# Kernel optimization log

Hardware: AMD Instinct MI355X
Metric: run time of the kernel (lower is better)

The kernel has to match this reference:

```python
import jax, jax.numpy as jnp
import numpy as np

B, F, V, D = 16384, 16, 100000, 16  # batch, n_fields, vocab, embed_dim; dims = F*D = 256
EPS = 1e-5


def _bn(x, g, b):
    # torch.nn.BatchNorm1d in training mode: biased batch variance
    m = x.mean(0)
    v = x.var(0)
    return g * (x - m) * jax.lax.rsqrt(v + EPS) + b


def setup_inputs() -> dict:
    ks = iter(jax.random.split(jax.random.key(0), 40))

    def rn(shape, s=0.05):
        return jax.random.normal(next(ks), shape, jnp.float32) * s

    return {
        "feat_ids": jax.random.randint(next(ks), (B, F), 0, V, jnp.int32),
        "domain_ids": jax.random.randint(next(ks), (B,), 0, 3, jnp.int32),
        "emb": rn((F, V, D), 0.1),
        "hW0": rn((256, 128)), "hb0": jnp.zeros(128), "hg0": jnp.ones(128), "hbe0": jnp.zeros(128),
        "hW1": rn((128, 64)), "hb1": jnp.zeros(64), "hg1": jnp.ones(64), "hbe1": jnp.zeros(64),
        "hW2": rn((64, 1024)), "hb2": jnp.zeros(1024), "hg2": jnp.ones(1024), "hbe2": jnp.zeros(1024),
        "cw": rn((3, 256)), "cb": jnp.zeros((3, 256)),
        "mW0": rn((256, 512)), "mb0": jnp.zeros(512), "mg0": jnp.ones(512), "mbe0": jnp.zeros(512),
        "mW1": rn((512, 256)), "mb1": jnp.zeros(256), "mg1": jnp.ones(256), "mbe1": jnp.zeros(256),
        "u0": rn((256, 32)), "u1": rn((32, 32)), "v0": rn((32, 32)), "v1": rn((32, 256)),
        "ab0": jnp.zeros(32), "ab1": jnp.zeros(256),
        "gamma1": jnp.ones(256), "bias1": jnp.zeros(256),
        "lw": rn((512,)), "lb": jnp.zeros(1),
    }


def _forward(feat_ids, emb, hW0, hb0, hg0, hbe0, hW1, hb1, hg1, hbe1,
             hW2, hb2, hg2, hbe2, cw, cb, mW0, mb0, mg0, mbe0,
             mW1, mb1, mg1, mbe1, u0, u1, v0, v1, ab0, ab1,
             gamma1, bias1, lw, lb):
    b, f = feat_ids.shape
    # EmbeddingLayer(squeeze_dim=True): per-field lookup then concat -> [B, F*D]
    e = emb[jnp.arange(f)[None, :], feat_ids].reshape(b, -1)
    h = e
    for W, bb, g, be in ((hW0, hb0, hg0, hbe0), (hW1, hb1, hg1, hbe1), (hW2, hb2, hg2, hbe2)):
        h = jax.nn.relu(_bn(h @ W + bb, g, be))
    k = u1.shape[0]
    H = h.reshape(b, k, k)  # [B, k, k]
    # CrossNetwork: x_{l+1} = x0 * (x_l . w_l) + b_l + x_l
    x = e
    for i in range(cw.shape[0]):
        x = e * (x @ cw[i])[:, None] + cb[i] + x
    cn_out = x  # [B, 256]
    m = e
    for W, bb, g, be in ((mW0, mb0, mg0, mbe0), (mW1, mb1, mg1, mbe1)):
        m = jax.nn.relu(_bn(m @ W + bb, g, be))
    # hyper low-rank adapter: einsum('mi,bij,jn->bmn') applied lazily so the
    # [B,256,32] per-sample weight is never materialized (associativity)
    t = jax.nn.sigmoid(jnp.einsum('bi,bij->bj', m @ u0, H) @ v0 + ab0)   # [B, 32]
    t = jnp.einsum('bi,bij->bj', t @ u1, H) @ v1 + ab1                    # [B, 256]
    mu = t.mean(0)
    var = t.var(0, ddof=1)  # torch.var default is unbiased
    m = gamma1 * (t - mu) / jnp.sqrt(var + EPS) + bias1 + m  # norm + residual
    y = jnp.concatenate([cn_out, m], axis=1) @ lw + lb[0]     # LR head
    # Every domain branch computes identical values (shared weights, full-batch
    # input, dropout p=0), so the torch.where domain-select is the identity.
    return jax.nn.sigmoid(y)  # [B]


def reference(feat_ids, domain_ids, emb, hW0, hb0, hg0, hbe0, hW1, hb1, hg1, hbe1,
              hW2, hb2, hg2, hbe2, cw, cb, mW0, mb0, mg0, mbe0,
              mW1, mb1, mg1, mbe1, u0, u1, v0, v1, ab0, ab1,
              gamma1, bias1, lw, lb):
    return _forward(feat_ids, emb, hW0, hb0, hg0, hbe0, hW1, hb1, hg1, hbe1,
                    hW2, hb2, hg2, hbe2, cw, cb, mW0, mb0, mg0, mbe0,
                    mW1, mb1, mg1, mbe1, u0, u1, v0, v1, ab0, ab1,
                    gamma1, bias1, lw, lb)
```

## Files before the change

### kernel.cpp

```cpp
#include <hip/hip_runtime.h>

typedef unsigned short u16;
typedef __attribute__((ext_vector_type(8))) short bf16x8;
typedef __attribute__((ext_vector_type(4))) float f32x4;
#define BATCH 16384

__device__ __forceinline__ float b2f(u16 u){ unsigned int i=((unsigned int)u)<<16; float f; __builtin_memcpy(&f,&i,4); return f; }
__device__ __forceinline__ u16 f2b(float f){ unsigned int x; __builtin_memcpy(&x,&f,4); unsigned int r=(x + 0x7fffu + ((x>>16)&1u))>>16; return (u16)r; }

__global__ __launch_bounds__(256) void zero_kernel(float* __restrict__ p, int n){
  int i = blockIdx.x*256 + threadIdx.x;
  if (i < n) p[i] = 0.f;
}

__global__ __launch_bounds__(256) void transpose_weights(const float* __restrict__ w0, const float* __restrict__ w1,
                                                         const float* __restrict__ w2, const float* __restrict__ w3,
                                                         const float* __restrict__ w4, const float* __restrict__ w5,
                                                         const float* __restrict__ w6,
                                                         u16* __restrict__ t0, u16* __restrict__ t1,
                                                         u16* __restrict__ t2, u16* __restrict__ t3,
                                                         u16* __restrict__ t4, u16* __restrict__ t5,
                                                         u16* __restrict__ t6){
  int b = blockIdx.x;
  if (b < 128){        int idx=(b-0)*256+threadIdx.x;    t0[idx]=f2b(w0[(idx%256)*128  + idx/256]); }
  else if (b < 160){   int idx=(b-128)*256+threadIdx.x;  t1[idx]=f2b(w1[(idx%128)*64   + idx/128]); }
  else if (b < 416){   int idx=(b-160)*256+threadIdx.x;  t2[idx]=f2b(w2[(idx%64)*1024  + idx/64]);  }
  else if (b < 928){   int idx=(b-416)*256+threadIdx.x;  t3[idx]=f2b(w3[(idx%256)*512  + idx/256]); }
  else if (b < 1440){  int idx=(b-928)*256+threadIdx.x;  t4[idx]=f2b(w4[(idx%512)*256  + idx/512]); }
  else if (b < 1472){  int idx=(b-1440)*256+threadIdx.x; t5[idx]=f2b(w5[(idx%256)*32   + idx/256]); }
  else {               int idx=(b-1472)*256+threadIdx.x; t6[idx]=f2b(w6[(idx%32)*256   + idx/32]);  }
}

__global__ __launch_bounds__(256) void gather_kernel(const int* __restrict__ ids,
                                                     const float* __restrict__ emb,
                                                     u16* __restrict__ e){
  int b = blockIdx.x; int tid = threadIdx.x;
  int f = tid >> 4, d = tid & 15;
  int id = ids[b*16 + f];
  e[(size_t)b*256 + tid] = f2b(emb[((size_t)f*100000 + (size_t)id)*16 + d]);
}

#define ASTR 40
__global__ __launch_bounds__(256) void gemm_mfma(const u16* __restrict__ A,
                                                 const u16* __restrict__ Wt,
                                                 const float* __restrict__ bias,
                                                 u16* __restrict__ C,
                                                 const float* __restrict__ ascale,
                                                 const float* __restrict__ ashift,
                                                 float* __restrict__ sums,
                                                 float* __restrict__ sumsq,
                                                 int N, int K){
  __shared__ u16 lds[64*ASTR*2];
  u16* As = lds;
  u16* Bs = lds + 64*ASTR;
  int tid = threadIdx.x;
  int n0 = blockIdx.x*64, m0 = blockIdx.y*64;
  int srow = tid >> 2, skoff = (tid & 3)*8;
  int lane = tid & 63, w = tid >> 6, quad = lane >> 4, m16 = lane & 15;
  f32x4 acc[4] = {};
  int ng = n0 + srow;
  for (int k0 = 0; k0 < K; k0 += 32){
    uint4 av = *(const uint4*)(A + (size_t)(m0+srow)*K + k0 + skoff);
    u16 at[8]; __builtin_memcpy(at, &av, 16);
    if (ascale != nullptr){
#pragma unroll
      for (int j=0;j<8;j++){
        float v = b2f(at[j]) * ascale[k0+skoff+j] + ashift[k0+skoff+j];
        at[j] = f2b(v > 0.f ? v : 0.f);
      }
    }
    __builtin_memcpy(&av, at, 16);
    *(uint4*)&As[srow*ASTR + skoff] = av;
    uint4 wv = make_uint4(0u,0u,0u,0u);
    if (ng < N) wv = *(const uint4*)(Wt + (size_t)ng*K + k0 + skoff);
    *(uint4*)&Bs[srow*ASTR + skoff] = wv;
    __syncthreads();
    bf16x8 bfrag = *(bf16x8*)&Bs[(w*16 + m16)*ASTR + quad*8];
#pragma unroll
    for (int mc=0;mc<4;mc++){
      bf16x8 afrag = *(bf16x8*)&As[(mc*16 + m16)*ASTR + quad*8];
      acc[mc] = __builtin_amdgcn_mfma_f32_16x16x32_bf16(afrag, bfrag, acc[mc], 0, 0, 0);
    }
    __syncthreads();
  }
  int cw = n0 + w*16 + m16;
  float bv = (bias != nullptr && cw < N) ? bias[cw] : 0.f;
  float cs = 0.f, cq = 0.f;
  u16* Cs = lds;
#pragma unroll
  for (int mc=0;mc<4;mc++)
#pragma unroll
    for (int r=0;r<4;r++){
      float v = acc[mc][r] + bv;
      cs += v; cq += v*v;
      Cs[(mc*16 + quad*4 + r)*72 + w*16 + m16] = f2b(v);
    }
  if (sums != nullptr){
    cs += __shfl_xor(cs, 16, 64); cs += __shfl_xor(cs, 32, 64);
    cq += __shfl_xor(cq, 16, 64); cq += __shfl_xor(cq, 32, 64);
    if (quad == 0 && cw < N){ atomicAdd(&sums[cw], cs); atomicAdd(&sumsq[cw], cq); }
  }
  __syncthreads();
  int row = tid >> 2, c4 = (tid & 3)*16;
  int cg = n0 + c4;
  if (cg < N){
    uint4 p0 = *(uint4*)&Cs[row*72 + c4];
    uint4 p1 = *(uint4*)&Cs[row*72 + c4 + 8];
    *(uint4*)(C + (size_t)(m0+row)*N + cg) = p0;
    *(uint4*)(C + (size_t)(m0+row)*N + cg + 8) = p1;
  }
}

__global__ void finalize_kernel(const float* __restrict__ sums, const float* __restrict__ sumsq,
                                const float* __restrict__ g, const float* __restrict__ be,
                                float* __restrict__ scale, float* __restrict__ shift,
                                int N, int unbiased){
  int c = blockIdx.x*256 + threadIdx.x;
  if (c >= N) return;
  float mean = sums[c] / (float)BATCH;
  float var;
  if (unbiased) var = (sumsq[c] - mean*mean*(float)BATCH) / (float)(BATCH-1);
  else          var = sumsq[c] / (float)BATCH - mean*mean;
  float sc = g[c] * rsqrtf(var + 1e-5f);
  scale[c] = sc;
  shift[c] = be[c] - mean * sc;
}

__global__ __launch_bounds__(256) void adapter_core(const u16* __restrict__ H,
                                                    const u16* __restrict__ P,
                                                    const float* __restrict__ v0,
                                                    const float* __restrict__ u1,
                                                    const float* __restrict__ ab0,
                                                    const float* __restrict__ hscale,
                                                    const float* __restrict__ hshift,
                                                    u16* __restrict__ Z2){
  __shared__ __align__(16) u16 Hs[8*1024];
  __shared__ float v0s[1024], u1s[1024];
  __shared__ float Ps[256], qs[256], t1s[256], ss[256];
  __shared__ float ab0s[32];
  int tid = threadIdx.x;
  int r = tid >> 5, j = tid & 31;
  size_t row0 = (size_t)blockIdx.x * 8;

  for (int k = tid; k < 8*1024; k += 256){
    int col = k & 1023;
    float v = b2f(H[row0*1024 + k]) * hscale[col] + hshift[col];
    Hs[k] = f2b(v > 0.f ? v : 0.f);
  }
  for (int k = tid; k < 1024; k += 256){ v0s[k] = v0[k]; u1s[k] = u1[k]; }
  if (tid < 32) ab0s[tid] = ab0[tid];
  Ps[tid] = b2f(P[row0*32 + tid]);
  __syncthreads();

  float acc = 0.f;
#pragma unroll
  for (int i=0;i<32;i++) acc += Ps[r*32+i] * b2f(Hs[r*1024 + i*32 + j]);
  qs[r*32+j] = acc;
  __syncthreads();

  acc = ab0s[j];
#pragma unroll
  for (int i=0;i<32;i++) acc += qs[r*32+i] * v0s[i*32+j];
  t1s[r*32+j] = 1.f / (1.f + __expf(-acc));
  __syncthreads();

  acc = 0.f;
#pragma unroll
  for (int i=0;i<32;i++) acc += t1s[r*32+i] * u1s[i*32+j];
  ss[r*32+j] = acc;
  __syncthreads();

  acc = 0.f;
#pragma unroll
  for (int i=0;i<32;i++) acc += ss[r*32+i] * b2f(Hs[r*1024 + i*32 + j]);
  Z2[(row0 + r)*32 + j] = f2b(acc);
}

__global__ __launch_bounds__(256) void final_kernel(const u16* __restrict__ e,
                                                    const float* __restrict__ cw,
                                                    const float* __restrict__ cb,
                                                    const u16* __restrict__ t,
                                                    const u16* __restrict__ mo,
                                                    const float* __restrict__ tS,
                                                    const float* __restrict__ tB,
                                                    const float* __restrict__ mS,
                                                    const float* __restrict__ mB,
                                                    const float* __restrict__ lw,
                                                    const float* __restrict__ lb,
                                                    float* __restrict__ out){
  int wave = threadIdx.x >> 6, lane = threadIdx.x & 63;
  int b = blockIdx.x*4 + wave;
  int n4 = lane*4;
  ushort4 ev = *(const ushort4*)(e + (size_t)b*256 + n4);
  float ec[4] = { b2f(ev.x), b2f(ev.y), b2f(ev.z), b2f(ev.w) };
  float x[4]  = { ec[0], ec[1], ec[2], ec[3] };
  for (int i=0;i<3;i++){
    float p = 0.f;
#pragma unroll
    for (int q=0;q<4;q++) p += x[q] * cw[i*256 + n4 + q];
#pragma unroll
    for (int o=1;o<64;o<<=1) p += __shfl_xor(p, o, 64);
#pragma unroll
    for (int q=0;q<4;q++) x[q] = ec[q]*p + cb[i*256 + n4 + q] + x[q];
  }
  ushort4 tv = *(const ushort4*)(t  + (size_t)b*256 + n4);
  ushort4 mv = *(const ushort4*)(mo + (size_t)b*256 + n4);
  float ta[4] = { b2f(tv.x), b2f(tv.y), b2f(tv.z), b2f(tv.w) };
  float ma[4] = { b2f(mv.x), b2f(mv.y), b2f(mv.z), b2f(mv.w) };
  float p = 0.f;
#pragma unroll
  for (int q=0;q<4;q++){
    int n = n4 + q;
    p += x[q] * lw[n];
    float mr = ma[q]*mS[n] + mB[n];
    mr = mr > 0.f ? mr : 0.f;
    float mf = tS[n]*ta[q] + tB[n] + mr;
    p += mf * lw[256 + n];
  }
#pragma unroll
  for (int o=32;o>0;o>>=1) p += __shfl_down(p, o, 64);
  if (lane == 0){
    float y = p + lb[0];
    out[b] = 1.f / (1.f + __expf(-y));
  }
}

extern "C" void kernel_launch(void* const* d_in, const int* in_sizes, int n_in,
                              void* d_out, int out_size, void* d_ws, size_t ws_size,
                              hipStream_t stream) {
  const int B = BATCH;
  const int*   feat = (const int*)d_in[0];
  const float* emb  = (const float*)d_in[2];
  const float* hW0 = (const float*)d_in[3],  *hb0 = (const float*)d_in[4],  *hg0 = (const float*)d_in[5],  *hbe0 = (const float*)d_in[6];
  const float* hW1 = (const float*)d_in[7],  *hb1 = (const float*)d_in[8],  *hg1 = (const float*)d_in[9],  *hbe1 = (const float*)d_in[10];
  const float* hW2 = (const float*)d_in[11], *hb2 = (const float*)d_in[12], *hg2 = (const float*)d_in[13], *hbe2 = (const float*)d_in[14];
  const float* cw  = (const float*)d_in[15], *cb  = (const float*)d_in[16];
  const float* mW0 = (const float*)d_in[17], *mb0 = (const float*)d_in[18], *mg0 = (const float*)d_in[19], *mbe0 = (const float*)d_in[20];
  const float* mW1 = (const float*)d_in[21], *mb1 = (const float*)d_in[22], *mg1 = (const float*)d_in[23], *mbe1 = (const float*)d_in[24];
  const float* u0  = (const float*)d_in[25], *u1  = (const float*)d_in[26];
  const float* v0  = (const float*)d_in[27], *v1  = (const float*)d_in[28];
  const float* ab0 = (const float*)d_in[29], *ab1 = (const float*)d_in[30];
  const float* gamma1 = (const float*)d_in[31], *bias1 = (const float*)d_in[32];
  const float* lw  = (const float*)d_in[33], *lb = (const float*)d_in[34];
  float* out = (float*)d_out;

  char* base = (char*)d_ws;
  const size_t MB = 1024*1024;
  u16* H    = (u16*)(base);
  u16* e    = (u16*)(base + 32*MB);
  u16* Y0   = (u16*)(base + 40*MB);
  u16* Y1   = (u16*)(base + 44*MB);
  u16* M0   = (u16*)(base + 40*MB);
  u16* T    = (u16*)(base + 40*MB);
  u16* P    = (u16*)(base + 48*MB);
  u16* Z2   = (u16*)(base + 49*MB);
  u16* Mout = (u16*)(base + 56*MB);
  u16* hW0t = (u16*)(base + 56*MB);
  u16* hW1t = hW0t + 32768;
  u16* hW2t = hW1t + 8192;
  u16* mW0t = hW2t + 65536;
  float* S  = (float*)(base + 64*MB);
  auto sums  = [&](int l){ return S + l*2048; };
  auto sumsq = [&](int l){ return S + l*2048 + 1024; };
  float* SS = S + 12288;
  auto scl = [&](int l){ return SS + l*2048; };
  auto shf = [&](int l){ return SS + l*2048 + 1024; };
  u16* mW1t = (u16*)(base + 64*MB + 112*1024);
  u16* u0t  = mW1t + 131072;
  u16* v1t  = u0t + 8192;

  zero_kernel<<<48, 256, 0, stream>>>(S, 12288);
  transpose_weights<<<1504, 256, 0, stream>>>(hW0, hW1, hW2, mW0, mW1, u0, v1,
                                              hW0t, hW1t, hW2t, mW0t, mW1t, u0t, v1t);
  gather_kernel<<<B, 256, 0, stream>>>(feat, emb, e);

  gemm_mfma<<<dim3(2, B/64), 256, 0, stream>>>(e,  hW0t, hb0, Y0, nullptr, nullptr, sums(0), sumsq(0), 128, 256);
  finalize_kernel<<<1, 256, 0, stream>>>(sums(0), sumsq(0), hg0, hbe0, scl(0), shf(0), 128, 0);

  gemm_mfma<<<dim3(1, B/64), 256, 0, stream>>>(Y0, hW1t, hb1, Y1, scl(0), shf(0), sums(1), sumsq(1), 64, 128);
  finalize_kernel<<<1, 256, 0, stream>>>(sums(1), sumsq(1), hg1, hbe1, scl(1), shf(1), 64, 0);

  gemm_mfma<<<dim3(16, B/64), 256, 0, stream>>>(Y1, hW2t, hb2, H, scl(1), shf(1), sums(2), sumsq(2), 1024, 64);
  finalize_kernel<<<4, 256, 0, stream>>>(sums(2), sumsq(2), hg2, hbe2, scl(2), shf(2), 1024, 0);

  gemm_mfma<<<dim3(8, B/64), 256, 0, stream>>>(e,  mW0t, mb0, M0, nullptr, nullptr, sums(3), sumsq(3), 512, 256);
  finalize_kernel<<<2, 256, 0, stream>>>(sums(3), sumsq(3), mg0, mbe0, scl(3), shf(3), 512, 0);

  gemm_mfma<<<dim3(4, B/64), 256, 0, stream>>>(M0, mW1t, mb1, Mout, scl(3), shf(3), sums(4), sumsq(4), 256, 512);
  finalize_kernel<<<1, 256, 0, stream>>>(sums(4), sumsq(4), mg1, mbe1, scl(4), shf(4), 256, 0);

  gemm_mfma<<<dim3(1, B/64), 256, 0, stream>>>(Mout, u0t, nullptr, P, scl(4), shf(4), nullptr, nullptr, 32, 256);
  adapter_core<<<B/8, 256, 0, stream>>>(H, P, v0, u1, ab0, scl(2), shf(2), Z2);
  gemm_mfma<<<dim3(4, B/64), 256, 0, stream>>>(Z2, v1t, ab1, T, nullptr, nullptr, sums(5), sumsq(5), 256, 32);
  finalize_kernel<<<1, 256, 0, stream>>>(sums(5), sumsq(5), gamma1, bias1, scl(5), shf(5), 256, 1);

  final_kernel<<<B/4, 256, 0, stream>>>(e, cw, cb, T, Mout, scl(5), shf(5), scl(4), shf(4), lw, lb, out);
}
```

Measured before the change: 371.2 us.

## Merge prep kernels and fold BN finalize into consumer kernels

Combines the zeroing, weight transpose and embedding gather into one prep kernel launch. Removes the separate BN finalize kernels by having each consumer (GEMM, adapter_core, final_kernel) compute the batch-norm scale and shift from the sums into LDS at block start. This cuts roughly eight kernel launches and their serialization gaps. In exchange, every block recomputes the per-channel stats, and the GEMM adds LDS use plus a barrier.

```diff
diff --git a/kernel.cpp b/kernel.cpp
--- a/kernel.cpp
+++ b/kernel.cpp
@@ -8,36 +8,38 @@
 __device__ __forceinline__ float b2f(u16 u){ unsigned int i=((unsigned int)u)<<16; float f; __builtin_memcpy(&f,&i,4); return f; }
 __device__ __forceinline__ u16 f2b(float f){ unsigned int x; __builtin_memcpy(&x,&f,4); unsigned int r=(x + 0x7fffu + ((x>>16)&1u))>>16; return (u16)r; }
 
-__global__ __launch_bounds__(256) void zero_kernel(float* __restrict__ p, int n){
-  int i = blockIdx.x*256 + threadIdx.x;
-  if (i < n) p[i] = 0.f;
-}
-
-__global__ __launch_bounds__(256) void transpose_weights(const float* __restrict__ w0, const float* __restrict__ w1,
-                                                         const float* __restrict__ w2, const float* __restrict__ w3,
-                                                         const float* __restrict__ w4, const float* __restrict__ w5,
-                                                         const float* __restrict__ w6,
-                                                         u16* __restrict__ t0, u16* __restrict__ t1,
-                                                         u16* __restrict__ t2, u16* __restrict__ t3,
-                                                         u16* __restrict__ t4, u16* __restrict__ t5,
-                                                         u16* __restrict__ t6){
-  int b = blockIdx.x;
-  if (b < 128){        int idx=(b-0)*256+threadIdx.x;    t0[idx]=f2b(w0[(idx%256)*128  + idx/256]); }
-  else if (b < 160){   int idx=(b-128)*256+threadIdx.x;  t1[idx]=f2b(w1[(idx%128)*64   + idx/128]); }
-  else if (b < 416){   int idx=(b-160)*256+threadIdx.x;  t2[idx]=f2b(w2[(idx%64)*1024  + idx/64]);  }
-  else if (b < 928){   int idx=(b-416)*256+threadIdx.x;  t3[idx]=f2b(w3[(idx%256)*512  + idx/256]); }
-  else if (b < 1440){  int idx=(b-928)*256+threadIdx.x;  t4[idx]=f2b(w4[(idx%512)*256  + idx/512]); }
-  else if (b < 1472){  int idx=(b-1440)*256+threadIdx.x; t5[idx]=f2b(w5[(idx%256)*32   + idx/256]); }
-  else {               int idx=(b-1472)*256+threadIdx.x; t6[idx]=f2b(w6[(idx%32)*256   + idx/32]);  }
-}
-
-__global__ __launch_bounds__(256) void gather_kernel(const int* __restrict__ ids,
-                                                     const float* __restrict__ emb,
-                                                     u16* __restrict__ e){
-  int b = blockIdx.x; int tid = threadIdx.x;
-  int f = tid >> 4, d = tid & 15;
-  int id = ids[b*16 + f];
-  e[(size_t)b*256 + tid] = f2b(emb[((size_t)f*100000 + (size_t)id)*16 + d]);
+__global__ __launch_bounds__(256) void prep_kernel(float* __restrict__ S,
+                                                   const float* __restrict__ w0, const float* __restrict__ w1,
+                                                   const float* __restrict__ w2, const float* __restrict__ w3,
+                                                   const float* __restrict__ w4, const float* __restrict__ w5,
+                                                   const float* __restrict__ w6,
+                                                   u16* __restrict__ t0, u16* __restrict__ t1,
+                                                   u16* __restrict__ t2, u16* __restrict__ t3,
+                                                   u16* __restrict__ t4, u16* __restrict__ t5,
+                                                   u16* __restrict__ t6,
+                                                   const int* __restrict__ ids,
+                                                   const float* __restrict__ emb,
+                                                   u16* __restrict__ e){
+  int blk = blockIdx.x;
+  if (blk < 48){
+    int i = blk*256 + threadIdx.x;
+    if (i < 12288) S[i] = 0.f;
+  } else if (blk < 1552){
+    int b = blk - 48;
+    if (b < 128){        int idx=(b-0)*256+threadIdx.x;    t0[idx]=f2b(w0[(idx%256)*128  + idx/256]); }
+    else if (b < 160){   int idx=(b-128)*256+threadIdx.x;  t1[idx]=f2b(w1[(idx%128)*64   + idx/128]); }
+    else if (b < 416){   int idx=(b-160)*256+threadIdx.x;  t2[idx]=f2b(w2[(idx%64)*1024  + idx/64]);  }
+    else if (b < 928){   int idx=(b-416)*256+threadIdx.x;  t3[idx]=f2b(w3[(idx%256)*512  + idx/256]); }
+    else if (b < 1440){  int idx=(b-928)*256+threadIdx.x;  t4[idx]=f2b(w4[(idx%512)*256  + idx/512]); }
+    else if (b < 1472){  int idx=(b-1440)*256+threadIdx.x; t5[idx]=f2b(w5[(idx%256)*32   + idx/256]); }
+    else {               int idx=(b-1472)*256+threadIdx.x; t6[idx]=f2b(w6[(idx%32)*256   + idx/32]);  }
+  } else {
+    int b = blk - 1552;
+    int tid = threadIdx.x;
+    int f = tid >> 4, d = tid & 15;
+    int id = ids[b*16 + f];
+    e[(size_t)b*256 + tid] = f2b(emb[((size_t)f*100000 + (size_t)id)*16 + d]);
+  }
 }
 
 #define ASTR 40
@@ -45,27 +47,40 @@
                                                  const u16* __restrict__ Wt,
                                                  const float* __restrict__ bias,
                                                  u16* __restrict__ C,
-                                                 const float* __restrict__ ascale,
-                                                 const float* __restrict__ ashift,
+                                                 const float* __restrict__ asums,
+                                                 const float* __restrict__ asumsq,
+                                                 const float* __restrict__ ag,
+                                                 const float* __restrict__ abe,
                                                  float* __restrict__ sums,
                                                  float* __restrict__ sumsq,
                                                  int N, int K){
   __shared__ u16 lds[64*ASTR*2];
+  __shared__ float bnS[512], bnB[512];
   u16* As = lds;
   u16* Bs = lds + 64*ASTR;
   int tid = threadIdx.x;
   int n0 = blockIdx.x*64, m0 = blockIdx.y*64;
   int srow = tid >> 2, skoff = (tid & 3)*8;
   int lane = tid & 63, w = tid >> 6, quad = lane >> 4, m16 = lane & 15;
+  if (asums != nullptr){
+    for (int k = tid; k < K; k += 256){
+      float mean = asums[k] * (1.f/(float)BATCH);
+      float var  = asumsq[k] * (1.f/(float)BATCH) - mean*mean;
+      float sc   = ag[k] * rsqrtf(var + 1e-5f);
+      bnS[k] = sc;
+      bnB[k] = abe[k] - mean*sc;
+    }
+    __syncthreads();
+  }
   f32x4 acc[4] = {};
   int ng = n0 + srow;
   for (int k0 = 0; k0 < K; k0 += 32){
     uint4 av = *(const uint4*)(A + (size_t)(m0+srow)*K + k0 + skoff);
     u16 at[8]; __builtin_memcpy(at, &av, 16);
-    if (ascale != nullptr){
+    if (asums != nullptr){
 #pragma unroll
       for (int j=0;j<8;j++){
-        float v = b2f(at[j]) * ascale[k0+skoff+j] + ashift[k0+skoff+j];
+        float v = b2f(at[j]) * bnS[k0+skoff+j] + bnB[k0+skoff+j];
         at[j] = f2b(v > 0.f ? v : 0.f);
       }
     }
@@ -111,30 +126,18 @@
   }
 }
 
-__global__ void finalize_kernel(const float* __restrict__ sums, const float* __restrict__ sumsq,
-                                const float* __restrict__ g, const float* __restrict__ be,
-                                float* __restrict__ scale, float* __restrict__ shift,
-                                int N, int unbiased){
-  int c = blockIdx.x*256 + threadIdx.x;
-  if (c >= N) return;
-  float mean = sums[c] / (float)BATCH;
-  float var;
-  if (unbiased) var = (sumsq[c] - mean*mean*(float)BATCH) / (float)(BATCH-1);
-  else          var = sumsq[c] / (float)BATCH - mean*mean;
-  float sc = g[c] * rsqrtf(var + 1e-5f);
-  scale[c] = sc;
-  shift[c] = be[c] - mean * sc;
-}
-
 __global__ __launch_bounds__(256) void adapter_core(const u16* __restrict__ H,
                                                     const u16* __restrict__ P,
                                                     const float* __restrict__ v0,
                                                     const float* __restrict__ u1,
                                                     const float* __restrict__ ab0,
-                                                    const float* __restrict__ hscale,
-                                                    const float* __restrict__ hshift,
+                                                    const float* __restrict__ hsums,
+                                                    const float* __restrict__ hsumsq,
+                                                    const float* __restrict__ hg,
+                                                    const float* __restrict__ hbe,
                                                     u16* __restrict__ Z2){
   __shared__ __align__(16) u16 Hs[8*1024];
+  __shared__ float bnS[1024], bnB[1024];
   __shared__ float v0s[1024], u1s[1024];
   __shared__ float Ps[256], qs[256], t1s[256], ss[256];
   __shared__ float ab0s[32];
@@ -142,14 +145,22 @@
   int r = tid >> 5, j = tid & 31;
   size_t row0 = (size_t)blockIdx.x * 8;
 
+  for (int k = tid; k < 1024; k += 256){
+    float mean = hsums[k] * (1.f/(float)BATCH);
+    float var  = hsumsq[k] * (1.f/(float)BATCH) - mean*mean;
+    float sc   = hg[k] * rsqrtf(var + 1e-5f);
+    bnS[k] = sc;
+    bnB[k] = hbe[k] - mean*sc;
+    v0s[k] = v0[k]; u1s[k] = u1[k];
+  }
+  if (tid < 32) ab0s[tid] = ab0[tid];
+  Ps[tid] = b2f(P[row0*32 + tid]);
+  __syncthreads();
   for (int k = tid; k < 8*1024; k += 256){
     int col = k & 1023;
-    float v = b2f(H[row0*1024 + k]) * hscale[col] + hshift[col];
+    float v = b2f(H[row0*1024 + k]) * bnS[col] + bnB[col];
     Hs[k] = f2b(v > 0.f ? v : 0.f);
   }
-  for (int k = tid; k < 1024; k += 256){ v0s[k] = v0[k]; u1s[k] = u1[k]; }
-  if (tid < 32) ab0s[tid] = ab0[tid];
-  Ps[tid] = b2f(P[row0*32 + tid]);
   __syncthreads();
 
   float acc = 0.f;
@@ -181,14 +192,32 @@
                                                     const float* __restrict__ cb,
                                                     const u16* __restrict__ t,
                                                     const u16* __restrict__ mo,
-                                                    const float* __restrict__ tS,
-                                                    const float* __restrict__ tB,
-                                                    const float* __restrict__ mS,
-                                                    const float* __restrict__ mB,
+                                                    const float* __restrict__ tsums,
+                                                    const float* __restrict__ tsumsq,
+                                                    const float* __restrict__ tg,
+                                                    const float* __restrict__ tbe,
+                                                    const float* __restrict__ msums,
+                                                    const float* __restrict__ msumsq,
+                                                    const float* __restrict__ mg,
+                                                    const float* __restrict__ mbe,
                                                     const float* __restrict__ lw,
                                                     const float* __restrict__ lb,
                                                     float* __restrict__ out){
-  int wave = threadIdx.x >> 6, lane = threadIdx.x & 63;
+  __shared__ float tS[256], tB[256], mS[256], mB[256];
+  int tid = threadIdx.x;
+  {
+    int c = tid;
+    float mean = tsums[c] * (1.f/(float)BATCH);
+    float var  = (tsumsq[c] - mean*mean*(float)BATCH) * (1.f/(float)(BATCH-1));
+    float sc   = tg[c] * rsqrtf(var + 1e-5f);
+    tS[c] = sc; tB[c] = tbe[c] - mean*sc;
+    float mmean = msums[c] * (1.f/(float)BATCH);
+    float mvar  = msumsq[c] * (1.f/(float)BATCH) - mmean*mmean;
+    float msc   = mg[c] * rsqrtf(mvar + 1e-5f);
+    mS[c] = msc; mB[c] = mbe[c] - mmean*msc;
+  }
+  __syncthreads();
+  int wave = tid >> 6, lane = tid & 63;
   int b = blockIdx.x*4 + wave;
   int n4 = lane*4;
   ushort4 ev = *(const ushort4*)(e + (size_t)b*256 + n4);
@@ -262,37 +291,34 @@
   float* S  = (float*)(base + 64*MB);
   auto sums  = [&](int l){ return S + l*2048; };
   auto sumsq = [&](int l){ return S + l*2048 + 1024; };
-  float* SS = S + 12288;
-  auto scl = [&](int l){ return SS + l*2048; };
-  auto shf = [&](int l){ return SS + l*2048 + 1024; };
-  u16* mW1t = (u16*)(base + 64*MB + 112*1024);
+  u16* mW1t = (u16*)(base + 64*MB + 64*1024);
   u16* u0t  = mW1t + 131072;
   u16* v1t  = u0t + 8192;
 
-  zero_kernel<<<48, 256, 0, stream>>>(S, 12288);
-  transpose_weights<<<1504, 256, 0, stream>>>(hW0, hW1, hW2, mW0, mW1, u0, v1,
-                                              hW0t, hW1t, hW2t, mW0t, mW1t, u0t, v1t);
-  gather_kernel<<<B, 256, 0, stream>>>(feat, emb, e);
-
-  gemm_mfma<<<dim3(2, B/64), 256, 0, stream>>>(e,  hW0t, hb0, Y0, nullptr, nullptr, sums(0), sumsq(0), 128, 256);
-  finalize_kernel<<<1, 256, 0, stream>>>(sums(0), sumsq(0), hg0, hbe0, scl(0), shf(0), 128, 0);
-
-  gemm_mfma<<<dim3(1, B/64), 256, 0, stream>>>(Y0, hW1t, hb1, Y1, scl(0), shf(0), sums(1), sumsq(1), 64, 128);
-  finalize_kernel<<<1, 256, 0, stream>>>(sums(1), sumsq(1), hg1, hbe1, scl(1), shf(1), 64, 0);
-
-  gemm_mfma<<<dim3(16, B/64), 256, 0, stream>>>(Y1, hW2t, hb2, H, scl(1), shf(1), sums(2), sumsq(2), 1024, 64);
-  finalize_kernel<<<4, 256, 0, stream>>>(sums(2), sumsq(2), hg2, hbe2, scl(2), shf(2), 1024, 0);
-
-  gemm_mfma<<<dim3(8, B/64), 256, 0, stream>>>(e,  mW0t, mb0, M0, nullptr, nullptr, sums(3), sumsq(3), 512, 256);
-  finalize_kernel<<<2, 256, 0, stream>>>(sums(3), sumsq(3), mg0, mbe0, scl(3), shf(3), 512, 0);
-
-  gemm_mfma<<<dim3(4, B/64), 256, 0, stream>>>(M0, mW1t, mb1, Mout, scl(3), shf(3), sums(4), sumsq(4), 256, 512);
-  finalize_kernel<<<1, 256, 0, stream>>>(sums(4), sumsq(4), mg1, mbe1, scl(4), shf(4), 256, 0);
-
-  gemm_mfma<<<dim3(1, B/64), 256, 0, stream>>>(Mout, u0t, nullptr, P, scl(4), shf(4), nullptr, nullptr, 32, 256);
-  adapter_core<<<B/8, 256, 0, stream>>>(H, P, v0, u1, ab0, scl(2), shf(2), Z2);
-  gemm_mfma<<<dim3(4, B/64), 256, 0, stream>>>(Z2, v1t, ab1, T, nullptr, nullptr, sums(5), sumsq(5), 256, 32);
-  finalize_kernel<<<1, 256, 0, stream>>>(sums(5), sumsq(5), gamma1, bias1, scl(5), shf(5), 256, 1);
-
-  final_kernel<<<B/4, 256, 0, stream>>>(e, cw, cb, T, Mout, scl(5), shf(5), scl(4), shf(4), lw, lb, out);
-}
+  prep_kernel<<<17936, 256, 0, stream>>>(S, hW0, hW1, hW2, mW0, mW1, u0, v1,
+                                         hW0t, hW1t, hW2t, mW0t, mW1t, u0t, v1t,
+                                         feat, emb, e);
+
+  gemm_mfma<<<dim3(2, B/64), 256, 0, stream>>>(e,  hW0t, hb0, Y0,
+      nullptr, nullptr, nullptr, nullptr, sums(0), sumsq(0), 128, 256);
+  gemm_mfma<<<dim3(1, B/64), 256, 0, stream>>>(Y0, hW1t, hb1, Y1,
+      sums(0), sumsq(0), hg0, hbe0, sums(1), sumsq(1), 64, 128);
+  gemm_mfma<<<dim3(16, B/64), 256, 0, stream>>>(Y1, hW2t, hb2, H,
+      sums(1), sumsq(1), hg1, hbe1, sums(2), sumsq(2), 1024, 64);
+
+  gemm_mfma<<<dim3(8, B/64), 256, 0, stream>>>(e,  mW0t, mb0, M0,
+      nullptr, nullptr, nullptr, nullptr, sums(3), sumsq(3), 512, 256);
+  gemm_mfma<<<dim3(4, B/64), 256, 0, stream>>>(M0, mW1t, mb1, Mout,
+      sums(3), sumsq(3), mg0, mbe0, sums(4), sumsq(4), 256, 512);
+
+  gemm_mfma<<<dim3(1, B/64), 256, 0, stream>>>(Mout, u0t, nullptr, P,
+      sums(4), sumsq(4), mg1, mbe1, nullptr, nullptr, 32, 256);
+  adapter_core<<<B/8, 256, 0, stream>>>(H, P, v0, u1, ab0,
+      sums(2), sumsq(2), hg2, hbe2, Z2);
+  gemm_mfma<<<dim3(4, B/64), 256, 0, stream>>>(Z2, v1t, ab1, T,
+      nullptr, nullptr, nullptr, nullptr, sums(5), sumsq(5), 256, 32);
+
+  final_kernel<<<B/4, 256, 0, stream>>>(e, cw, cb, T, Mout,
+      sums(5), sumsq(5), gamma1, bias1,
+      sums(4), sumsq(4), mg1, mbe1, lw, lb, out);
+}
```

Result: faster. 357.1 us (-3.8%).
